# Kernel optimization log

Measured on AMD Instinct MI355X. Metric: run time of the kernel, lower is better.

The kernel has to match this reference:

```python
import jax, jax.numpy as jnp
import numpy as np

EPS = 1e-5

def _layer_norm(x, gamma, beta):
    m = jnp.mean(x, axis=-1, keepdims=True)
    v = jnp.mean(jnp.square(x - m), axis=-1, keepdims=True)
    return (x - m) * jax.lax.rsqrt(v + EPS) * gamma + beta

def setup_inputs() -> dict:
    key = jax.random.key(0)
    ks = jax.random.split(key, 6)
    B, D, H = 4096, 1024, 1024
    s = 1.0 / np.sqrt(H)
    return {
        "inputs": jax.random.normal(ks[0], (B, D), jnp.float32),
        "hx": jax.random.normal(ks[1], (B, H), jnp.float32),
        "cx": jax.random.normal(ks[2], (B, H), jnp.float32),
        "w_ih": jax.random.uniform(ks[3], (4 * H, D), jnp.float32, -s, s),
        "w_hh": jax.random.uniform(ks[4], (4 * H, H), jnp.float32, -s, s),
        "b_hh": jax.random.uniform(ks[5], (4 * H,), jnp.float32, -s, s),
        "g_ih": jnp.ones((4 * H,), jnp.float32),
        "beta_ih": jnp.zeros((4 * H,), jnp.float32),
        "g_hh": jnp.ones((4 * H,), jnp.float32),
        "beta_hh": jnp.zeros((4 * H,), jnp.float32),
        "g_ho": jnp.ones((H,), jnp.float32),
        "beta_ho": jnp.zeros((H,), jnp.float32),
    }

def reference(inputs, hx, cx, w_ih, w_hh, b_hh, g_ih, beta_ih, g_hh, beta_hh, g_ho, beta_ho):
    # i2h: [B, 4H] (no input bias used in original forward)
    i2h = inputs @ w_ih.T
    h2h = hx @ w_hh.T + b_hh
    gates = _layer_norm(i2h, g_ih, beta_ih) + _layer_norm(h2h, g_hh, beta_hh)
    i, f, o, g = jnp.split(gates, 4, axis=1)  # torch chunk order: i, f, o, g
    cy = jax.nn.sigmoid(f) * cx + jax.nn.sigmoid(i) * jnp.tanh(g)
    hy = jax.nn.sigmoid(o) * _layer_norm(jnp.tanh(cy), g_ho, beta_ho)
    # Dropout(0.1) is identity in eval / deterministic reference
    return hy, cy
```

## Files before the change

kernel.cpp:

```cpp
#include <hip/hip_runtime.h>
#include <hip/hip_bf16.h>
#include <stdint.h>

typedef __attribute__((ext_vector_type(8))) short bf16x8;
typedef __attribute__((ext_vector_type(4))) float f32x4;

#define LN_EPS 1e-5f
#define KP 1056
#define GNT 33

__device__ inline unsigned f2bf(float f) {
    unsigned u = __builtin_bit_cast(unsigned, f);
    u += 0x7fffu + ((u >> 16) & 1u);
    return u >> 16;
}
__device__ inline float bf2f(unsigned u) {
    return __builtin_bit_cast(float, u << 16);
}
__device__ inline float sigf(float x) {
    return 1.0f / (1.0f + __expf(-x));
}
__device__ inline float tanh_fast(float x) {
    return __builtin_fmaf(2.0f, 1.0f / (1.0f + __expf(-2.0f * x)), -1.0f);
}
__device__ inline float wred(float v) {
#pragma unroll
    for (int o = 32; o > 0; o >>= 1) v += __shfl_xor(v, o);
    return v;
}
__device__ inline void gload_lds16(const void* g, void* l) {
    __builtin_amdgcn_global_load_lds(
        (const __attribute__((address_space(1))) void*)g,
        (__attribute__((address_space(3))) void*)l, 16, 0, 0);
}

__global__ __launch_bounds__(256) void cast_aug(
    const float* __restrict__ inputs, const float* __restrict__ hx,
    const float* __restrict__ w_ih,   const float* __restrict__ w_hh,
    const float* __restrict__ b_hh,
    unsigned short* __restrict__ Abf, unsigned short* __restrict__ Hbf,
    unsigned short* __restrict__ Wih, unsigned short* __restrict__ Whh)
{
    const int CPR = 132;
    const int PERREG = 4096 * CPR;
    int j = blockIdx.x * blockDim.x + threadIdx.x;
    const int r = j / PERREG;
    if (r >= 4) return;
    const int rem = j - r * PERREG;
    const int row = rem / CPR;
    const int c8  = rem - row * CPR;

    const float* src; unsigned short* dst;
    switch (r) {
        case 0: src = inputs; dst = Abf; break;
        case 1: src = hx;     dst = Hbf; break;
        case 2: src = w_ih;   dst = Wih; break;
        default: src = w_hh;  dst = Whh; break;
    }

    uint4 v;
    if (c8 < 128) {
        const float4* sp = reinterpret_cast<const float4*>(src + (size_t)row * 1024 + c8 * 8);
        float4 a = sp[0], b = sp[1];
        v.x = f2bf(a.x) | (f2bf(a.y) << 16);
        v.y = f2bf(a.z) | (f2bf(a.w) << 16);
        v.z = f2bf(b.x) | (f2bf(b.y) << 16);
        v.w = f2bf(b.z) | (f2bf(b.w) << 16);
    } else {
        v.x = v.y = v.z = v.w = 0u;
        if (c8 == 128) {
            if (r == 1) v.x = 0x3F80u;
            else if (r == 3) v.x = f2bf(b_hh[row]);
        }
    }
    *reinterpret_cast<uint4*>(dst + (size_t)row * KP + c8 * 8) = v;
}

__global__ __launch_bounds__(512) void gemm8p(
    const unsigned short* __restrict__ Aa, const unsigned short* __restrict__ Ba, unsigned short* __restrict__ Ca,
    const unsigned short* __restrict__ Ab, const unsigned short* __restrict__ Bb, unsigned short* __restrict__ Cb,
    float2* __restrict__ P,
    int N, int Bn)
{
    __shared__ __attribute__((aligned(16))) short lds[65536];
    short* ldsA = lds;
    short* ldsB = lds + 32768;

    const int gx  = gridDim.x;
    const int gxy = gx * gridDim.y;
    int bid = (blockIdx.z * gridDim.y + blockIdx.y) * gx + blockIdx.x;
    const int cpx = (gxy * gridDim.z) >> 3;
    int swz = (bid & 7) * cpx + (bid >> 3);
    const int z  = swz / gxy;
    const int r2 = swz - z * gxy;
    const int by = r2 / gx;
    const int bx = r2 - by * gx;

    const unsigned short* __restrict__ A = z ? Ab : Aa;
    const unsigned short* __restrict__ B = z ? Bb : Ba;
    unsigned short* __restrict__ C = z ? Cb : Ca;
    const int brow = by * 256, bcol = bx * 256;

    const int t    = threadIdx.x;
    const int lane = t & 63, w = t >> 6;
    const int wr = w >> 2, wc = w & 3;
    const int lr = lane & 15, kc = lane >> 4;

    const int ci0 = t, ci1 = t + 512;
    const int r0 = ci0 >> 2, l0 = (ci0 & 3) ^ ((r0 >> 1) & 3);
    const int r1 = ci1 >> 2, l1 = (ci1 & 3) ^ ((r1 >> 1) & 3);
    const int gA0 = (brow + r0) * KP + l0 * 8;
    const int gA1 = (brow + r1) * KP + l1 * 8;
    const int gB0 = (bcol + r0) * KP + l0 * 8;
    const int gB1 = (bcol + r1) * KP + l1 * 8;
    const int d0 = ci0 * 8, d1 = ci1 * 8;

#define STAGE_A(u) { const int so_ = ((u) & 3) * 8192; \
    gload_lds16(A + gA0 + (u) * 32, ldsA + so_ + d0);  \
    gload_lds16(A + gA1 + (u) * 32, ldsA + so_ + d1); }
#define STAGE_B(u) { const int so_ = ((u) & 3) * 8192; \
    gload_lds16(B + gB0 + (u) * 32, ldsB + so_ + d0);  \
    gload_lds16(B + gB1 + (u) * 32, ldsB + so_ + d1); }

    int offW[8], offX[4];
#pragma unroll
    for (int f = 0; f < 8; ++f) {
        int r = wr * 128 + f * 16 + lr;
        offW[f] = r * 32 + ((kc ^ ((r >> 1) & 3)) * 8);
    }
#pragma unroll
    for (int n = 0; n < 4; ++n) {
        int r = wc * 64 + n * 16 + lr;
        offX[n] = r * 32 + ((kc ^ ((r >> 1) & 3)) * 8);
    }

    f32x4 acc[8][4];
#pragma unroll
    for (int i = 0; i < 8; ++i)
#pragma unroll
        for (int j = 0; j < 4; ++j)
            acc[i][j] = (f32x4){0.f, 0.f, 0.f, 0.f};

    STAGE_A(0); STAGE_B(0); STAGE_A(1); STAGE_B(1); STAGE_A(2);
    asm volatile("s_waitcnt vmcnt(6)" ::: "memory");
    __builtin_amdgcn_s_barrier();

#pragma unroll 4
    for (int T = 0; T < GNT; ++T) {
        const int so = (T & 3) * 8192;
        bf16x8 w0, w1, w2, w3, x0, x1, x2, x3;

        w0 = *(const bf16x8*)&ldsB[so + offW[0]];
        w1 = *(const bf16x8*)&ldsB[so + offW[1]];
        w2 = *(const bf16x8*)&ldsB[so + offW[2]];
        w3 = *(const bf16x8*)&ldsB[so + offW[3]];
        x0 = *(const bf16x8*)&ldsA[so + offX[0]];
        x1 = *(const bf16x8*)&ldsA[so + offX[1]];
        x2 = *(const bf16x8*)&ldsA[so + offX[2]];
        x3 = *(const bf16x8*)&ldsA[so + offX[3]];
        if (T + 2 < GNT) STAGE_B(T + 2);
        __builtin_amdgcn_s_barrier();
        asm volatile("s_waitcnt lgkmcnt(0)" ::: "memory");
        __builtin_amdgcn_sched_barrier(0);
        __builtin_amdgcn_s_setprio(1);
        acc[0][0] = __builtin_amdgcn_mfma_f32_16x16x32_bf16(w0, x0, acc[0][0], 0, 0, 0);
        acc[0][1] = __builtin_amdgcn_mfma_f32_16x16x32_bf16(w0, x1, acc[0][1], 0, 0, 0);
        acc[0][2] = __builtin_amdgcn_mfma_f32_16x16x32_bf16(w0, x2, acc[0][2], 0, 0, 0);
        acc[0][3] = __builtin_amdgcn_mfma_f32_16x16x32_bf16(w0, x3, acc[0][3], 0, 0, 0);
        acc[1][0] = __builtin_amdgcn_mfma_f32_16x16x32_bf16(w1, x0, acc[1][0], 0, 0, 0);
        acc[1][1] = __builtin_amdgcn_mfma_f32_16x16x32_bf16(w1, x1, acc[1][1], 0, 0, 0);
        acc[1][2] = __builtin_amdgcn_mfma_f32_16x16x32_bf16(w1, x2, acc[1][2], 0, 0, 0);
        acc[1][3] = __builtin_amdgcn_mfma_f32_16x16x32_bf16(w1, x3, acc[1][3], 0, 0, 0);
        acc[2][0] = __builtin_amdgcn_mfma_f32_16x16x32_bf16(w2, x0, acc[2][0], 0, 0, 0);
        acc[2][1] = __builtin_amdgcn_mfma_f32_16x16x32_bf16(w2, x1, acc[2][1], 0, 0, 0);
        acc[2][2] = __builtin_amdgcn_mfma_f32_16x16x32_bf16(w2, x2, acc[2][2], 0, 0, 0);
        acc[2][3] = __builtin_amdgcn_mfma_f32_16x16x32_bf16(w2, x3, acc[2][3], 0, 0, 0);
        acc[3][0] = __builtin_amdgcn_mfma_f32_16x16x32_bf16(w3, x0, acc[3][0], 0, 0, 0);
        acc[3][1] = __builtin_amdgcn_mfma_f32_16x16x32_bf16(w3, x1, acc[3][1], 0, 0, 0);
        acc[3][2] = __builtin_amdgcn_mfma_f32_16x16x32_bf16(w3, x2, acc[3][2], 0, 0, 0);
        acc[3][3] = __builtin_amdgcn_mfma_f32_16x16x32_bf16(w3, x3, acc[3][3], 0, 0, 0);
        __builtin_amdgcn_s_setprio(0);
        __builtin_amdgcn_s_barrier();

        w0 = *(const bf16x8*)&ldsB[so + offW[4]];
        w1 = *(const bf16x8*)&ldsB[so + offW[5]];
        w2 = *(const bf16x8*)&ldsB[so + offW[6]];
        w3 = *(const bf16x8*)&ldsB[so + offW[7]];
        if (T + 3 < GNT) STAGE_A(T + 3);
        __builtin_amdgcn_s_barrier();
        asm volatile("s_waitcnt lgkmcnt(0)" ::: "memory");
        __builtin_amdgcn_sched_barrier(0);
        __builtin_amdgcn_s_setprio(1);
        acc[4][0] = __builtin_amdgcn_mfma_f32_16x16x32_bf16(w0, x0, acc[4][0], 0, 0, 0);
        acc[4][1] = __builtin_amdgcn_mfma_f32_16x16x32_bf16(w0, x1, acc[4][1], 0, 0, 0);
        acc[4][2] = __builtin_amdgcn_mfma_f32_16x16x32_bf16(w0, x2, acc[4][2], 0, 0, 0);
        acc[4][3] = __builtin_amdgcn_mfma_f32_16x16x32_bf16(w0, x3, acc[4][3], 0, 0, 0);
        acc[5][0] = __builtin_amdgcn_mfma_f32_16x16x32_bf16(w1, x0, acc[5][0], 0, 0, 0);
        acc[5][1] = __builtin_amdgcn_mfma_f32_16x16x32_bf16(w1, x1, acc[5][1], 0, 0, 0);
        acc[5][2] = __builtin_amdgcn_mfma_f32_16x16x32_bf16(w1, x2, acc[5][2], 0, 0, 0);
        acc[5][3] = __builtin_amdgcn_mfma_f32_16x16x32_bf16(w1, x3, acc[5][3], 0, 0, 0);
        acc[6][0] = __builtin_amdgcn_mfma_f32_16x16x32_bf16(w2, x0, acc[6][0], 0, 0, 0);
        acc[6][1] = __builtin_amdgcn_mfma_f32_16x16x32_bf16(w2, x1, acc[6][1], 0, 0, 0);
        acc[6][2] = __builtin_amdgcn_mfma_f32_16x16x32_bf16(w2, x2, acc[6][2], 0, 0, 0);
        acc[6][3] = __builtin_amdgcn_mfma_f32_16x16x32_bf16(w2, x3, acc[6][3], 0, 0, 0);
        acc[7][0] = __builtin_amdgcn_mfma_f32_16x16x32_bf16(w3, x0, acc[7][0], 0, 0, 0);
        acc[7][1] = __builtin_amdgcn_mfma_f32_16x16x32_bf16(w3, x1, acc[7][1], 0, 0, 0);
        acc[7][2] = __builtin_amdgcn_mfma_f32_16x16x32_bf16(w3, x2, acc[7][2], 0, 0, 0);
        acc[7][3] = __builtin_amdgcn_mfma_f32_16x16x32_bf16(w3, x3, acc[7][3], 0, 0, 0);
        __builtin_amdgcn_s_setprio(0);
        if (T < GNT - 3)      { asm volatile("s_waitcnt vmcnt(6)" ::: "memory"); }
        else if (T == GNT - 3){ asm volatile("s_waitcnt vmcnt(4)" ::: "memory"); }
        else if (T == GNT - 2){ asm volatile("s_waitcnt vmcnt(0)" ::: "memory"); }
        __builtin_amdgcn_s_barrier();
    }

    const int gc0 = bcol + wr * 128 + kc * 4;
    const int mr0 = brow + wc * 64 + lr;

    float s[4] = {0.f, 0.f, 0.f, 0.f}, q[4] = {0.f, 0.f, 0.f, 0.f};
#pragma unroll
    for (int f = 0; f < 8; ++f) {
#pragma unroll
        for (int n = 0; n < 4; ++n) {
            float a0 = acc[f][n][0], a1 = acc[f][n][1];
            float a2 = acc[f][n][2], a3 = acc[f][n][3];
            s[n] += (a0 + a1) + (a2 + a3);
            q[n] += __builtin_fmaf(a0, a0, a1 * a1) + __builtin_fmaf(a2, a2, a3 * a3);
            unsigned u0 = f2bf(a0), u1 = f2bf(a1), u2 = f2bf(a2), u3 = f2bf(a3);
            uint2 pk; pk.x = u0 | (u1 << 16); pk.y = u2 | (u3 << 16);
            *reinterpret_cast<uint2*>(&C[(size_t)(mr0 + n * 16) * N + gc0 + f * 16]) = pk;
        }
    }
#pragma unroll
    for (int n = 0; n < 4; ++n) {
        s[n] += __shfl_xor(s[n], 16); s[n] += __shfl_xor(s[n], 32);
        q[n] += __shfl_xor(q[n], 16); q[n] += __shfl_xor(q[n], 32);
    }
    if (kc == 0) {
#pragma unroll
        for (int n = 0; n < 4; ++n) {
            float2 pr; pr.x = s[n]; pr.y = q[n];
            P[(size_t)(z * Bn + mr0 + n * 16) * 32 + bx * 2 + wr] = pr;
        }
    }
#undef STAGE_A
#undef STAGE_B
}

__global__ __launch_bounds__(256) void ln_lstm(
    const unsigned short* __restrict__ i2h,
    const unsigned short* __restrict__ h2h,
    const float* __restrict__ cx,
    const float2* __restrict__ P,
    const float* __restrict__ g_ih, const float* __restrict__ be_ih,
    const float* __restrict__ g_hh, const float* __restrict__ be_hh,
    const float* __restrict__ g_ho, const float* __restrict__ be_ho,
    float* __restrict__ hy, float* __restrict__ cy, int H, int B)
{
    const int b = blockIdx.x;
    const int t = threadIdx.x;
    const int lane = t & 63;
    const int wave = t >> 6;
    const int H4 = 4 * H;
    const int h0 = t * 4;

    const unsigned short* xi = i2h + (size_t)b * H4;
    const unsigned short* xh = h2h + (size_t)b * H4;

    __shared__ float red[4][2];
    __shared__ float st[4];

    if (wave == 0) {
        const int half = lane >> 5;
        float2 v = P[((size_t)half * B + b) * 32 + (lane & 31)];
        v.x += __shfl_xor(v.x, 1);  v.y += __shfl_xor(v.y, 1);
        v.x += __shfl_xor(v.x, 2);  v.y += __shfl_xor(v.y, 2);
        v.x += __shfl_xor(v.x, 4);  v.y += __shfl_xor(v.y, 4);
        v.x += __shfl_xor(v.x, 8);  v.y += __shfl_xor(v.y, 8);
        v.x += __shfl_xor(v.x, 16); v.y += __shfl_xor(v.y, 16);
        if ((lane & 31) == 0) {
            const float inv4H = 1.0f / (float)H4;
            float m = v.x * inv4H;
            float r = rsqrtf(v.y * inv4H - m * m + LN_EPS);
            st[half * 2]     = m;
            st[half * 2 + 1] = r;
        }
    }
    __syncthreads();
    const float mI = st[0], rI = st[1], mH = st[2], rH = st[3];

    float gate[4][4];
#pragma unroll
    for (int q = 0; q < 4; ++q) {
        const int j = q * H + h0;
        ushort4 vi = *reinterpret_cast<const ushort4*>(&xi[j]);
        ushort4 vh = *reinterpret_cast<const ushort4*>(&xh[j]);
        float4 gi = *reinterpret_cast<const float4*>(&g_ih[j]);
        float4 bi = *reinterpret_cast<const float4*>(&be_ih[j]);
        float4 gh = *reinterpret_cast<const float4*>(&g_hh[j]);
        float4 bh = *reinterpret_cast<const float4*>(&be_hh[j]);
        gate[q][0] = (bf2f(vi.x) - mI) * rI * gi.x + bi.x + (bf2f(vh.x) - mH) * rH * gh.x + bh.x;
        gate[q][1] = (bf2f(vi.y) - mI) * rI * gi.y + bi.y + (bf2f(vh.y) - mH) * rH * gh.y + bh.y;
        gate[q][2] = (bf2f(vi.z) - mI) * rI * gi.z + bi.z + (bf2f(vh.z) - mH) * rH * gh.z + bh.z;
        gate[q][3] = (bf2f(vi.w) - mI) * rI * gi.w + bi.w + (bf2f(vh.w) - mH) * rH * gh.w + bh.w;
    }

    float4 cxv = *reinterpret_cast<const float4*>(&cx[(size_t)b * H + h0]);
    float cvals[4] = {cxv.x, cxv.y, cxv.z, cxv.w};
    float tv[4], ov[4];
    float s2 = 0.f, q2 = 0.f;
    float4 cyv;
#pragma unroll
    for (int k = 0; k < 4; ++k) {
        float c = sigf(gate[1][k]) * cvals[k] + sigf(gate[0][k]) * tanh_fast(gate[3][k]);
        ((float*)&cyv)[k] = c;
        float tc = tanh_fast(c);
        tv[k] = tc; ov[k] = sigf(gate[2][k]);
        s2 += tc; q2 += tc * tc;
    }
    *reinterpret_cast<float4*>(&cy[(size_t)b * H + h0]) = cyv;

    s2 = wred(s2); q2 = wred(q2);
    if (lane == 0) { red[wave][0] = s2; red[wave][1] = q2; }
    __syncthreads();
    float S2 = red[0][0] + red[1][0] + red[2][0] + red[3][0];
    float Q2 = red[0][1] + red[1][1] + red[2][1] + red[3][1];
    const float invH = 1.0f / (float)H;
    float mt = S2 * invH;
    float rt = rsqrtf(Q2 * invH - mt * mt + LN_EPS);

    float4 go = *reinterpret_cast<const float4*>(&g_ho[h0]);
    float4 bo = *reinterpret_cast<const float4*>(&be_ho[h0]);
    float4 hyv;
    hyv.x = ov[0] * ((tv[0] - mt) * rt * go.x + bo.x);
    hyv.y = ov[1] * ((tv[1] - mt) * rt * go.y + bo.y);
    hyv.z = ov[2] * ((tv[2] - mt) * rt * go.z + bo.z);
    hyv.w = ov[3] * ((tv[3] - mt) * rt * go.w + bo.w);
    *reinterpret_cast<float4*>(&hy[(size_t)b * H + h0]) = hyv;
}

extern "C" void kernel_launch(void* const* d_in, const int* in_sizes, int n_in,
                              void* d_out, int out_size, void* d_ws, size_t ws_size,
                              hipStream_t stream) {
    const float* inputs  = (const float*)d_in[0];
    const float* hx      = (const float*)d_in[1];
    const float* cx      = (const float*)d_in[2];
    const float* w_ih    = (const float*)d_in[3];
    const float* w_hh    = (const float*)d_in[4];
    const float* b_hh    = (const float*)d_in[5];
    const float* g_ih    = (const float*)d_in[6];
    const float* beta_ih = (const float*)d_in[7];
    const float* g_hh    = (const float*)d_in[8];
    const float* beta_hh = (const float*)d_in[9];
    const float* g_ho    = (const float*)d_in[10];
    const float* beta_ho = (const float*)d_in[11];

    const int H  = in_sizes[10];
    const int B  = in_sizes[1] / H;
    const int H4 = 4 * H;

    uint8_t* ws = (uint8_t*)d_ws;
    size_t off = 0;
    unsigned short* Abf = (unsigned short*)(ws + off); off += (size_t)B * KP * 2;
    unsigned short* Hbf = (unsigned short*)(ws + off); off += (size_t)B * KP * 2;
    unsigned short* Wih = (unsigned short*)(ws + off); off += (size_t)H4 * KP * 2;
    unsigned short* Whh = (unsigned short*)(ws + off); off += (size_t)H4 * KP * 2;
    unsigned short* i2hb = (unsigned short*)(ws + off); off += (size_t)B * H4 * 2;
    unsigned short* h2hb = (unsigned short*)(ws + off); off += (size_t)B * H4 * 2;
    float2* P   = (float2*)(ws + off); off += (size_t)2 * B * 32 * sizeof(float2);

    float* hy  = (float*)d_out;
    float* cyo = (float*)d_out + (size_t)B * H;

    {
        const int tot = 4 * 4096 * 132;
        cast_aug<<<(tot + 255) / 256, 256, 0, stream>>>(
            inputs, hx, w_ih, w_hh, b_hh, Abf, Hbf, Wih, Whh);
    }

    {
        dim3 grid(H4 / 256, B / 256, 2);
        gemm8p<<<grid, 512, 0, stream>>>(Abf, Wih, i2hb, Hbf, Whh, h2hb, P, H4, B);
    }

    ln_lstm<<<B, 256, 0, stream>>>(i2hb, h2hb, cx, P,
                                   g_ih, beta_ih, g_hh, beta_hh, g_ho, beta_ho,
                                   hy, cyo, H, B);
}
```

Measured before the change: 123.7 us.

## Shrink GEMM tile to 128x256 with double buffering for higher occupancy

The fused dual GEMM tile shrinks from 256x256 to 128 rows by 256 gates per block. Each wave now holds a 4x4 accumulator grid instead of 8x4. The LDS ring drops from four stages to two, cutting LDS use from 128KB to 48KB, and launch bounds request 4 blocks per CU. The goal is more concurrent blocks and smaller register pressure to hide latency. In exchange, arithmetic intensity per tile is lower and prefetch depth is shallower, with a full vmcnt(0) wait each iteration. The partial LayerNorm statistics layout widens to 64 slots per row, and the LN kernel reduction is adjusted to match.

```diff
diff --git a/kernel.cpp b/kernel.cpp
--- a/kernel.cpp
+++ b/kernel.cpp
@@ -76,15 +76,15 @@
     *reinterpret_cast<uint4*>(dst + (size_t)row * KP + c8 * 8) = v;
 }
 
-__global__ __launch_bounds__(512) void gemm8p(
+__global__ __launch_bounds__(512, 4) void gemmr2(
     const unsigned short* __restrict__ Aa, const unsigned short* __restrict__ Ba, unsigned short* __restrict__ Ca,
     const unsigned short* __restrict__ Ab, const unsigned short* __restrict__ Bb, unsigned short* __restrict__ Cb,
     float2* __restrict__ P,
     int N, int Bn)
 {
-    __shared__ __attribute__((aligned(16))) short lds[65536];
-    short* ldsA = lds;
-    short* ldsB = lds + 32768;
+    __shared__ __attribute__((aligned(16))) short lds[24576];
+    short* ldsW = lds;
+    short* ldsX = lds + 16384;
 
     const int gx  = gridDim.x;
     const int gxy = gx * gridDim.y;
@@ -96,70 +96,65 @@
     const int by = r2 / gx;
     const int bx = r2 - by * gx;
 
-    const unsigned short* __restrict__ A = z ? Ab : Aa;
-    const unsigned short* __restrict__ B = z ? Bb : Ba;
+    const unsigned short* __restrict__ X = z ? Ab : Aa;
+    const unsigned short* __restrict__ W = z ? Bb : Ba;
     unsigned short* __restrict__ C = z ? Cb : Ca;
-    const int brow = by * 256, bcol = bx * 256;
+    const int brow = by * 128, bcol = bx * 256;
 
     const int t    = threadIdx.x;
     const int lane = t & 63, w = t >> 6;
-    const int wr = w >> 2, wc = w & 3;
+    const int wg = w & 3, wb = w >> 2;
     const int lr = lane & 15, kc = lane >> 4;
 
-    const int ci0 = t, ci1 = t + 512;
-    const int r0 = ci0 >> 2, l0 = (ci0 & 3) ^ ((r0 >> 1) & 3);
-    const int r1 = ci1 >> 2, l1 = (ci1 & 3) ^ ((r1 >> 1) & 3);
-    const int gA0 = (brow + r0) * KP + l0 * 8;
-    const int gA1 = (brow + r1) * KP + l1 * 8;
-    const int gB0 = (bcol + r0) * KP + l0 * 8;
-    const int gB1 = (bcol + r1) * KP + l1 * 8;
-    const int d0 = ci0 * 8, d1 = ci1 * 8;
-
-#define STAGE_A(u) { const int so_ = ((u) & 3) * 8192; \
-    gload_lds16(A + gA0 + (u) * 32, ldsA + so_ + d0);  \
-    gload_lds16(A + gA1 + (u) * 32, ldsA + so_ + d1); }
-#define STAGE_B(u) { const int so_ = ((u) & 3) * 8192; \
-    gload_lds16(B + gB0 + (u) * 32, ldsB + so_ + d0);  \
-    gload_lds16(B + gB1 + (u) * 32, ldsB + so_ + d1); }
-
-    int offW[8], offX[4];
-#pragma unroll
-    for (int f = 0; f < 8; ++f) {
-        int r = wr * 128 + f * 16 + lr;
+    const int ciW0 = t, ciW1 = t + 512;
+    const int rW0 = ciW0 >> 2, lW0 = (ciW0 & 3) ^ ((rW0 >> 1) & 3);
+    const int rW1 = ciW1 >> 2, lW1 = (ciW1 & 3) ^ ((rW1 >> 1) & 3);
+    const int rX  = t >> 2,    lX  = (t & 3) ^ ((rX >> 1) & 3);
+    const int gW0 = (bcol + rW0) * KP + lW0 * 8;
+    const int gW1 = (bcol + rW1) * KP + lW1 * 8;
+    const int gX  = (brow + rX) * KP + lX * 8;
+    const int dW0 = ciW0 * 8, dW1 = ciW1 * 8, dX = t * 8;
+
+#define STAGE(u) { const int sW_ = ((u) & 1) * 8192, sX_ = ((u) & 1) * 4096; \
+    gload_lds16(W + gW0 + (u) * 32, ldsW + sW_ + dW0); \
+    gload_lds16(W + gW1 + (u) * 32, ldsW + sW_ + dW1); \
+    gload_lds16(X + gX  + (u) * 32, ldsX + sX_ + dX); }
+
+    int offW[4], offX[4];
+#pragma unroll
+    for (int f = 0; f < 4; ++f) {
+        int r = wg * 64 + f * 16 + lr;
         offW[f] = r * 32 + ((kc ^ ((r >> 1) & 3)) * 8);
     }
 #pragma unroll
     for (int n = 0; n < 4; ++n) {
-        int r = wc * 64 + n * 16 + lr;
+        int r = wb * 64 + n * 16 + lr;
         offX[n] = r * 32 + ((kc ^ ((r >> 1) & 3)) * 8);
     }
 
-    f32x4 acc[8][4];
-#pragma unroll
-    for (int i = 0; i < 8; ++i)
+    f32x4 acc[4][4];
+#pragma unroll
+    for (int i = 0; i < 4; ++i)
 #pragma unroll
         for (int j = 0; j < 4; ++j)
             acc[i][j] = (f32x4){0.f, 0.f, 0.f, 0.f};
 
-    STAGE_A(0); STAGE_B(0); STAGE_A(1); STAGE_B(1); STAGE_A(2);
-    asm volatile("s_waitcnt vmcnt(6)" ::: "memory");
+    STAGE(0);
+    asm volatile("s_waitcnt vmcnt(0)" ::: "memory");
     __builtin_amdgcn_s_barrier();
 
-#pragma unroll 4
+#pragma unroll 2
     for (int T = 0; T < GNT; ++T) {
-        const int so = (T & 3) * 8192;
-        bf16x8 w0, w1, w2, w3, x0, x1, x2, x3;
-
-        w0 = *(const bf16x8*)&ldsB[so + offW[0]];
-        w1 = *(const bf16x8*)&ldsB[so + offW[1]];
-        w2 = *(const bf16x8*)&ldsB[so + offW[2]];
-        w3 = *(const bf16x8*)&ldsB[so + offW[3]];
-        x0 = *(const bf16x8*)&ldsA[so + offX[0]];
-        x1 = *(const bf16x8*)&ldsA[so + offX[1]];
-        x2 = *(const bf16x8*)&ldsA[so + offX[2]];
-        x3 = *(const bf16x8*)&ldsA[so + offX[3]];
-        if (T + 2 < GNT) STAGE_B(T + 2);
-        __builtin_amdgcn_s_barrier();
+        const int sW = (T & 1) * 8192, sX = (T & 1) * 4096;
+        if (T + 1 < GNT) STAGE(T + 1);
+        bf16x8 w0 = *(const bf16x8*)&ldsW[sW + offW[0]];
+        bf16x8 w1 = *(const bf16x8*)&ldsW[sW + offW[1]];
+        bf16x8 w2 = *(const bf16x8*)&ldsW[sW + offW[2]];
+        bf16x8 w3 = *(const bf16x8*)&ldsW[sW + offW[3]];
+        bf16x8 x0 = *(const bf16x8*)&ldsX[sX + offX[0]];
+        bf16x8 x1 = *(const bf16x8*)&ldsX[sX + offX[1]];
+        bf16x8 x2 = *(const bf16x8*)&ldsX[sX + offX[2]];
+        bf16x8 x3 = *(const bf16x8*)&ldsX[sX + offX[3]];
         asm volatile("s_waitcnt lgkmcnt(0)" ::: "memory");
         __builtin_amdgcn_sched_barrier(0);
         __builtin_amdgcn_s_setprio(1);
@@ -180,46 +175,16 @@
         acc[3][2] = __builtin_amdgcn_mfma_f32_16x16x32_bf16(w3, x2, acc[3][2], 0, 0, 0);
         acc[3][3] = __builtin_amdgcn_mfma_f32_16x16x32_bf16(w3, x3, acc[3][3], 0, 0, 0);
         __builtin_amdgcn_s_setprio(0);
+        if (T + 1 < GNT) { asm volatile("s_waitcnt vmcnt(0)" ::: "memory"); }
         __builtin_amdgcn_s_barrier();
-
-        w0 = *(const bf16x8*)&ldsB[so + offW[4]];
-        w1 = *(const bf16x8*)&ldsB[so + offW[5]];
-        w2 = *(const bf16x8*)&ldsB[so + offW[6]];
-        w3 = *(const bf16x8*)&ldsB[so + offW[7]];
-        if (T + 3 < GNT) STAGE_A(T + 3);
-        __builtin_amdgcn_s_barrier();
-        asm volatile("s_waitcnt lgkmcnt(0)" ::: "memory");
-        __builtin_amdgcn_sched_barrier(0);
-        __builtin_amdgcn_s_setprio(1);
-        acc[4][0] = __builtin_amdgcn_mfma_f32_16x16x32_bf16(w0, x0, acc[4][0], 0, 0, 0);
-        acc[4][1] = __builtin_amdgcn_mfma_f32_16x16x32_bf16(w0, x1, acc[4][1], 0, 0, 0);
-        acc[4][2] = __builtin_amdgcn_mfma_f32_16x16x32_bf16(w0, x2, acc[4][2], 0, 0, 0);
-        acc[4][3] = __builtin_amdgcn_mfma_f32_16x16x32_bf16(w0, x3, acc[4][3], 0, 0, 0);
-        acc[5][0] = __builtin_amdgcn_mfma_f32_16x16x32_bf16(w1, x0, acc[5][0], 0, 0, 0);
-        acc[5][1] = __builtin_amdgcn_mfma_f32_16x16x32_bf16(w1, x1, acc[5][1], 0, 0, 0);
-        acc[5][2] = __builtin_amdgcn_mfma_f32_16x16x32_bf16(w1, x2, acc[5][2], 0, 0, 0);
-        acc[5][3] = __builtin_amdgcn_mfma_f32_16x16x32_bf16(w1, x3, acc[5][3], 0, 0, 0);
-        acc[6][0] = __builtin_amdgcn_mfma_f32_16x16x32_bf16(w2, x0, acc[6][0], 0, 0, 0);
-        acc[6][1] = __builtin_amdgcn_mfma_f32_16x16x32_bf16(w2, x1, acc[6][1], 0, 0, 0);
-        acc[6][2] = __builtin_amdgcn_mfma_f32_16x16x32_bf16(w2, x2, acc[6][2], 0, 0, 0);
-        acc[6][3] = __builtin_amdgcn_mfma_f32_16x16x32_bf16(w2, x3, acc[6][3], 0, 0, 0);
-        acc[7][0] = __builtin_amdgcn_mfma_f32_16x16x32_bf16(w3, x0, acc[7][0], 0, 0, 0);
-        acc[7][1] = __builtin_amdgcn_mfma_f32_16x16x32_bf16(w3, x1, acc[7][1], 0, 0, 0);
-        acc[7][2] = __builtin_amdgcn_mfma_f32_16x16x32_bf16(w3, x2, acc[7][2], 0, 0, 0);
-        acc[7][3] = __builtin_amdgcn_mfma_f32_16x16x32_bf16(w3, x3, acc[7][3], 0, 0, 0);
-        __builtin_amdgcn_s_setprio(0);
-        if (T < GNT - 3)      { asm volatile("s_waitcnt vmcnt(6)" ::: "memory"); }
-        else if (T == GNT - 3){ asm volatile("s_waitcnt vmcnt(4)" ::: "memory"); }
-        else if (T == GNT - 2){ asm volatile("s_waitcnt vmcnt(0)" ::: "memory"); }
-        __builtin_amdgcn_s_barrier();
-    }
-
-    const int gc0 = bcol + wr * 128 + kc * 4;
-    const int mr0 = brow + wc * 64 + lr;
+    }
+
+    const int gate0 = bcol + wg * 64 + kc * 4;
+    const int row0  = brow + wb * 64 + lr;
 
     float s[4] = {0.f, 0.f, 0.f, 0.f}, q[4] = {0.f, 0.f, 0.f, 0.f};
 #pragma unroll
-    for (int f = 0; f < 8; ++f) {
+    for (int f = 0; f < 4; ++f) {
 #pragma unroll
         for (int n = 0; n < 4; ++n) {
             float a0 = acc[f][n][0], a1 = acc[f][n][1];
@@ -228,7 +193,7 @@
             q[n] += __builtin_fmaf(a0, a0, a1 * a1) + __builtin_fmaf(a2, a2, a3 * a3);
             unsigned u0 = f2bf(a0), u1 = f2bf(a1), u2 = f2bf(a2), u3 = f2bf(a3);
             uint2 pk; pk.x = u0 | (u1 << 16); pk.y = u2 | (u3 << 16);
-            *reinterpret_cast<uint2*>(&C[(size_t)(mr0 + n * 16) * N + gc0 + f * 16]) = pk;
+            *reinterpret_cast<uint2*>(&C[(size_t)(row0 + n * 16) * N + gate0 + f * 16]) = pk;
         }
     }
 #pragma unroll
@@ -240,11 +205,10 @@
 #pragma unroll
         for (int n = 0; n < 4; ++n) {
             float2 pr; pr.x = s[n]; pr.y = q[n];
-            P[(size_t)(z * Bn + mr0 + n * 16) * 32 + bx * 2 + wr] = pr;
+            P[(size_t)(z * Bn + row0 + n * 16) * 64 + bx * 4 + wg] = pr;
         }
     }
-#undef STAGE_A
-#undef STAGE_B
+#undef STAGE
 }
 
 __global__ __launch_bounds__(256) void ln_lstm(
@@ -270,20 +234,20 @@
     __shared__ float red[4][2];
     __shared__ float st[4];
 
-    if (wave == 0) {
-        const int half = lane >> 5;
-        float2 v = P[((size_t)half * B + b) * 32 + (lane & 31)];
+    if (wave < 2) {
+        float2 v = P[((size_t)wave * B + b) * 64 + lane];
         v.x += __shfl_xor(v.x, 1);  v.y += __shfl_xor(v.y, 1);
         v.x += __shfl_xor(v.x, 2);  v.y += __shfl_xor(v.y, 2);
         v.x += __shfl_xor(v.x, 4);  v.y += __shfl_xor(v.y, 4);
         v.x += __shfl_xor(v.x, 8);  v.y += __shfl_xor(v.y, 8);
         v.x += __shfl_xor(v.x, 16); v.y += __shfl_xor(v.y, 16);
-        if ((lane & 31) == 0) {
+        v.x += __shfl_xor(v.x, 32); v.y += __shfl_xor(v.y, 32);
+        if (lane == 0) {
             const float inv4H = 1.0f / (float)H4;
             float m = v.x * inv4H;
             float r = rsqrtf(v.y * inv4H - m * m + LN_EPS);
-            st[half * 2]     = m;
-            st[half * 2 + 1] = r;
+            st[wave * 2]     = m;
+            st[wave * 2 + 1] = r;
         }
     }
     __syncthreads();
@@ -367,7 +331,7 @@
     unsigned short* Whh = (unsigned short*)(ws + off); off += (size_t)H4 * KP * 2;
     unsigned short* i2hb = (unsigned short*)(ws + off); off += (size_t)B * H4 * 2;
     unsigned short* h2hb = (unsigned short*)(ws + off); off += (size_t)B * H4 * 2;
-    float2* P   = (float2*)(ws + off); off += (size_t)2 * B * 32 * sizeof(float2);
+    float2* P   = (float2*)(ws + off); off += (size_t)2 * B * 64 * sizeof(float2);
 
     float* hy  = (float*)d_out;
     float* cyo = (float*)d_out + (size_t)B * H;
@@ -379,8 +343,8 @@
     }
 
     {
-        dim3 grid(H4 / 256, B / 256, 2);
-        gemm8p<<<grid, 512, 0, stream>>>(Abf, Wih, i2hb, Hbf, Whh, h2hb, P, H4, B);
+        dim3 grid(H4 / 256, B / 128, 2);
+        gemmr2<<<grid, 512, 0, stream>>>(Abf, Wih, i2hb, Hbf, Whh, h2hb, P, H4, B);
     }
 
     ln_lstm<<<B, 256, 0, stream>>>(i2hb, h2hb, cx, P,
```

After: 129.8 us. 1.05x slower.
